# Kernel tuning notes

Measured on AMD Instinct MI355X. Metric: run time of the kernel, lower is better.

## Reference

```python
import jax, jax.numpy as jnp
import numpy as np

N = 50000      # nodes
E = 800000     # edges (before self-loops)
F = 128        # num_features
H = 64         # hidden_channels
B = 512        # batch_size (num graphs)
NC = 10        # num_classes


def setup_inputs() -> dict:
    key = jax.random.key(0)
    ks = jax.random.split(key, 24)
    rn = lambda k, shp, s=0.05: jax.random.normal(k, shp, jnp.float32) * s
    inp = {}
    inp["x"] = jax.random.normal(ks[0], (N, F), jnp.float32)
    inp["edge_index"] = jax.random.randint(ks[1], (2, E), 0, N)
    inp["batch"] = jnp.sort(jax.random.randint(ks[2], (N,), 0, B))
    # GATConv1: in F -> 4 heads x H (concat)
    inp["W1"] = rn(ks[3], (F, 4 * H)); inp["a_src1"] = rn(ks[4], (4, H))
    inp["a_dst1"] = rn(ks[5], (4, H)); inp["b1"] = rn(ks[6], (4 * H,))
    # GATConv2: in 4H -> 1 head x 2H
    inp["W2"] = rn(ks[7], (4 * H, 2 * H)); inp["a_src2"] = rn(ks[8], (1, 2 * H))
    inp["a_dst2"] = rn(ks[9], (1, 2 * H)); inp["b2"] = rn(ks[10], (2 * H,))
    # GCNConv: in 2H -> H
    inp["Wg"] = rn(ks[11], (2 * H, H)); inp["bg"] = rn(ks[12], (H,))
    # BatchNorms (eval mode: running_mean=0, running_var=1)
    inp["bn1_g"] = 1.0 + rn(ks[13], (4 * H,)); inp["bn1_b"] = rn(ks[14], (4 * H,))
    inp["bn2_g"] = 1.0 + rn(ks[15], (2 * H,)); inp["bn2_b"] = rn(ks[16], (2 * H,))
    inp["bn3_g"] = 1.0 + rn(ks[17], (2 * H,)); inp["bn3_b"] = rn(ks[18], (2 * H,))
    inp["lin1_W"] = rn(ks[19], (H, 128)); inp["lin1_b"] = rn(ks[20], (128,))
    inp["lin2_W"] = rn(ks[21], (128, NC)); inp["lin2_b"] = rn(ks[22], (NC,))
    inp["batch_size"] = B
    return inp


def _gat(x, src, dst, W, a_s, a_d, b, n):
    """PyG GATConv (eval): project, edge attention (leaky_relu 0.2), dst-softmax, scatter."""
    heads, ch = a_s.shape
    h = (x @ W).reshape(n, heads, ch)                       # [N, heads, ch]
    sc_s = (h * a_s).sum(-1)                                # [N, heads]
    sc_d = (h * a_d).sum(-1)
    e = jax.nn.leaky_relu(sc_s[src] + sc_d[dst], 0.2)       # [E2, heads]
    m = jax.ops.segment_max(e, dst, num_segments=n)
    ee = jnp.exp(e - m[dst])
    s = jax.ops.segment_sum(ee, dst, num_segments=n)
    alpha = ee / (s[dst] + 1e-16)                           # edge softmax per dst
    out = jax.ops.segment_sum(h[src] * alpha[:, :, None], dst, num_segments=n)
    return out.reshape(n, heads * ch) + b


def _bn_eval(x, g, b, eps=1e-5):
    # BatchNorm1d eval with running_mean=0, running_var=1
    return x * (g / jnp.sqrt(1.0 + eps)) + b


def reference(x, edge_index, batch, W1, a_src1, a_dst1, b1, W2, a_src2, a_dst2, b2,
              Wg, bg, bn1_g, bn1_b, bn2_g, bn2_b, bn3_g, bn3_b,
              lin1_W, lin1_b, lin2_W, lin2_b, batch_size):
    n = x.shape[0]
    loop = jnp.arange(n)
    src = jnp.concatenate([edge_index[0], loop])            # add self-loops (PyG default)
    dst = jnp.concatenate([edge_index[1], loop])
    lrelu = lambda v: jax.nn.leaky_relu(v, 0.01)            # module's LeakyReLU()

    x1 = _bn_eval(lrelu(_gat(x, src, dst, W1, a_src1, a_dst1, b1, n)), bn1_g, bn1_b)
    x2 = _bn_eval(lrelu(_gat(x1, src, dst, W2, a_src2, a_dst2, b2, n)), bn2_g, bn2_b)

    # GCNConv with symmetric normalization over A + I
    deg = jax.ops.segment_sum(jnp.ones_like(dst, jnp.float32), dst, num_segments=n)
    dis = jnp.where(deg > 0, jax.lax.rsqrt(deg), 0.0)
    h = x2 @ Wg                                             # [N, H]
    msg = h[src] * (dis[src] * dis[dst])[:, None]
    x3 = lrelu(jax.ops.segment_sum(msg, dst, num_segments=n) + bg)

    # global_mean_pool over graphs (dropout is identity in eval)
    sums = jax.ops.segment_sum(x3, batch, num_segments=batch_size)
    cnt = jax.ops.segment_sum(jnp.ones((n,), jnp.float32), batch, num_segments=batch_size)
    pooled = sums / jnp.clip(cnt, 1.0)[:, None]             # [B, H]

    y = lrelu(_bn_eval(pooled @ lin1_W + lin1_b, bn3_g, bn3_b))
    return y @ lin2_W + lin2_b                              # [B, NC]
```

## Files before the change

### kernel.cpp

```cpp
#include <hip/hip_runtime.h>
#include <hip/hip_bf16.h>

#define NN  50000
#define EE  800000
#define NE2 850000
#define NB  512
#define NRT 3125
#define NSB 196
#define NEB ((NE2 + 255) / 256)

#define BN_RS 0.9999950000374997f

typedef __attribute__((ext_vector_type(8))) short short8;
typedef __attribute__((ext_vector_type(4))) float f32x4;

__device__ __forceinline__ float bf2f(__hip_bfloat16 v) { return __bfloat162float(v); }
__device__ __forceinline__ unsigned short f2b(float v) {
    __hip_bfloat16 b = __float2bfloat16(v);
    return *reinterpret_cast<unsigned short*>(&b);
}
__device__ __forceinline__ float u2f(unsigned short u) {
    union { unsigned u; float f; } c; c.u = ((unsigned)u) << 16; return c.f;
}
__device__ __forceinline__ float lrelu01(float v) { return v > 0.f ? v : 0.01f * v; }
__device__ __forceinline__ float lrelu02(float v) { return v > 0.f ? v : 0.2f * v; }

__device__ __forceinline__ void up2(unsigned u, float& lo, float& hi) {
    union { unsigned x; float f; } a, b;
    a.x = u << 16; b.x = u & 0xFFFF0000u;
    lo = a.f; hi = b.f;
}
__device__ __forceinline__ void acc8(float* acc, uint4 u, float e) {
    float lo, hi;
    up2(u.x, lo, hi); acc[0] = fmaf(lo, e, acc[0]); acc[1] = fmaf(hi, e, acc[1]);
    up2(u.y, lo, hi); acc[2] = fmaf(lo, e, acc[2]); acc[3] = fmaf(hi, e, acc[3]);
    up2(u.z, lo, hi); acc[4] = fmaf(lo, e, acc[4]); acc[5] = fmaf(hi, e, acc[5]);
    up2(u.w, lo, hi); acc[6] = fmaf(lo, e, acc[6]); acc[7] = fmaf(hi, e, acc[7]);
}
__device__ __forceinline__ unsigned packbf2(float lo, float hi) {
    return ((unsigned)f2b(hi) << 16) | (unsigned)f2b(lo);
}

__device__ __forceinline__ void edge_sd(const int* __restrict__ ei, int e, int& s, int& d) {
    if (e < EE) { s = ei[e]; d = ei[EE + e]; }
    else        { s = e - EE; d = e - EE; }
}

__device__ __forceinline__ float ldf(const void* p, int i, bool bf) {
    return bf ? bf2f(((const __hip_bfloat16*)p)[i]) : ((const float*)p)[i];
}

#define NSEG 20
#define WTOT 85578
#define XQUADS (NN * 32)
#define PREP_TOT (XQUADS + WTOT + 32768 + 32768 + 8192 + NE2)
struct SegArgs { const void* src[NSEG]; int off[NSEG]; };

__global__ __launch_bounds__(256) void prep_k(SegArgs a,
                                              const void* __restrict__ x_raw,
                                              ushort4* __restrict__ xb4,
                                              const void* __restrict__ W1r,
                                              const void* __restrict__ W2r,
                                              const void* __restrict__ Wgr,
                                              float* __restrict__ wf,
                                              unsigned short* __restrict__ W1t,
                                              unsigned short* __restrict__ W2t,
                                              unsigned short* __restrict__ Wgt,
                                              const int* __restrict__ ei,
                                              int* __restrict__ degi,
                                              int* __restrict__ flag) {
    __shared__ int cnt;
    int t = threadIdx.x;
    if (t == 0) cnt = 0;
    __syncthreads();
    {
        int c = 0;
        const unsigned* xw = (const unsigned*)x_raw;
#pragma unroll
        for (int k = 0; k < 4; ++k) {
            unsigned w = xw[t * 4 + k];
            unsigned ef = (w >> 7) & 0xFFu;
            if (ef >= 100u && ef <= 140u) c++;
        }
        atomicAdd(&cnt, c);
    }
    __syncthreads();
    bool bf = (cnt > 512);
    if (blockIdx.x == 0 && t == 0) *flag = bf ? 1 : 0;

    int i = blockIdx.x * 256 + t;
    if (i >= PREP_TOT) return;
    if (i < XQUADS) {
        ushort4 o;
        if (bf) o = ((const ushort4*)x_raw)[i];
        else {
            float4 v = ((const float4*)x_raw)[i];
            o.x = f2b(v.x); o.y = f2b(v.y); o.z = f2b(v.z); o.w = f2b(v.w);
        }
        xb4[i] = o;
        return;
    }
    i -= XQUADS;
    if (i < WTOT) {
        int s = 0;
#pragma unroll
        for (int k = 1; k < NSEG; ++k) if (i >= a.off[k]) s = k;
        wf[i] = ldf(a.src[s], i - a.off[s], bf);
        return;
    }
    i -= WTOT;
    if (i < 32768) {
        int n = i >> 7, k = i & 127;
        W1t[i] = f2b(ldf(W1r, k * 256 + n, bf));
        return;
    }
    i -= 32768;
    if (i < 32768) {
        int n = i >> 8, k = i & 255;
        W2t[i] = f2b(ldf(W2r, k * 128 + n, bf));
        return;
    }
    i -= 32768;
    if (i < 8192) {
        int n = i >> 7, k = i & 127;
        Wgt[i] = f2b(ldf(Wgr, k * 64 + n, bf));
        return;
    }
    i -= 8192;
    {
        int s, d; edge_sd(ei, i, s, d);
        atomicAdd(&degi[d], 1);
    }
}

__global__ __launch_bounds__(256) void pscan_k(const int* __restrict__ degi,
                                               int* __restrict__ incl, int* __restrict__ bsum) {
    __shared__ int tmp[256];
    int t = threadIdx.x;
    int i = blockIdx.x * 256 + t;
    int v = (i < NN) ? degi[i] : 0;
    tmp[t] = v;
    __syncthreads();
#pragma unroll
    for (int off = 1; off < 256; off <<= 1) {
        int u = (t >= off) ? tmp[t - off] : 0;
        __syncthreads();
        tmp[t] += u;
        __syncthreads();
    }
    if (i < NN) incl[i] = tmp[t];
    if (t == 255) bsum[blockIdx.x] = tmp[255];
}

__global__ __launch_bounds__(256) void bscan_k(int* __restrict__ bsum) {
    __shared__ int tmp[256];
    int t = threadIdx.x;
    tmp[t] = (t < NSB) ? bsum[t] : 0;
    __syncthreads();
#pragma unroll
    for (int off = 1; off < 256; off <<= 1) {
        int u = (t >= off) ? tmp[t - off] : 0;
        __syncthreads();
        tmp[t] += u;
        __syncthreads();
    }
    if (t < NSB) bsum[t] = tmp[t];
}

__global__ __launch_bounds__(256) void fscan_k(const int* __restrict__ degi,
                                               const int* __restrict__ incl,
                                               const int* __restrict__ bsum,
                                               const int* __restrict__ batch,
                                               int* __restrict__ row_ptr, int* __restrict__ cursor,
                                               float* __restrict__ dis, int* __restrict__ gstart) {
    int i = blockIdx.x * 256 + threadIdx.x;
    if (i <= NB) {
        int lo = 0, hi = NN;
        while (lo < hi) { int mid = (lo + hi) >> 1; if (batch[mid] < i) lo = mid + 1; else hi = mid; }
        gstart[i] = lo;
    }
    if (i >= NN) return;
    int dg = degi[i];
    int base = (blockIdx.x > 0) ? bsum[blockIdx.x - 1] : 0;
    int ex = base + incl[i] - dg;
    row_ptr[i] = ex; cursor[i] = ex;
    dis[i] = dg > 0 ? rsqrtf((float)dg) : 0.f;
    if (i == NN - 1) row_ptr[NN] = bsum[NSB - 1];
}

__global__ __launch_bounds__(256) void scatter_k(const int* __restrict__ ei,
                                                 int* __restrict__ cursor,
                                                 int* __restrict__ csr_src) {
    int e = blockIdx.x * 256 + threadIdx.x;
    if (e >= NE2) return;
    int s, d; edge_sd(ei, e, s, d);
    int pos = atomicAdd(&cursor[d], 1);
    csr_src[pos] = s;
}

__global__ __launch_bounds__(256) void mgemm1_k(const short* __restrict__ A,
                                                const short* __restrict__ Bt,
                                                unsigned short* __restrict__ C,
                                                const float* __restrict__ a_s,
                                                const float* __restrict__ a_d,
                                                float* __restrict__ sc_s,
                                                float* __restrict__ sc_d) {
    int wave = threadIdx.x >> 6, lane = threadIdx.x & 63;
    int cg = wave;
    int l15 = lane & 15, quad = lane >> 4;
    const short* bp = Bt + (size_t)(cg * 64 + l15) * 128 + quad * 8;
    short8 bfr[4][4];
#pragma unroll
    for (int j = 0; j < 4; ++j)
#pragma unroll
        for (int kk = 0; kk < 4; ++kk)
            bfr[j][kk] = *(const short8*)(bp + (size_t)j * 16 * 128 + kk * 32);
    float asv[4], adv[4];
#pragma unroll
    for (int j = 0; j < 4; ++j) {
        asv[j] = a_s[cg * 64 + j * 16 + l15];
        adv[j] = a_d[cg * 64 + j * 16 + l15];
    }
#pragma unroll
    for (int rtl = 0; rtl < 4; ++rtl) {
        int rt = blockIdx.x * 4 + rtl;
        if (rt >= NRT) break;
        const short* ap = A + (size_t)(rt * 16 + l15) * 128 + quad * 8;
        f32x4 acc[4] = {};
#pragma unroll
        for (int kk = 0; kk < 4; ++kk) {
            short8 a = *(const short8*)(ap + kk * 32);
#pragma unroll
            for (int j = 0; j < 4; ++j)
                acc[j] = __builtin_amdgcn_mfma_f32_16x16x32_bf16(a, bfr[j][kk], acc[j], 0, 0, 0);
        }
        float ss[4] = {0.f, 0.f, 0.f, 0.f}, sd[4] = {0.f, 0.f, 0.f, 0.f};
#pragma unroll
        for (int j = 0; j < 4; ++j) {
            int n = cg * 64 + j * 16 + l15;
#pragma unroll
            for (int r = 0; r < 4; ++r) {
                float v = acc[j][r];
                C[(size_t)(rt * 16 + quad * 4 + r) * 256 + n] = f2b(v);
                ss[r] = fmaf(v, asv[j], ss[r]);
                sd[r] = fmaf(v, adv[j], sd[r]);
            }
        }
#pragma unroll
        for (int off = 1; off < 16; off <<= 1) {
#pragma unroll
            for (int r = 0; r < 4; ++r) {
                ss[r] += __shfl_xor(ss[r], off);
                sd[r] += __shfl_xor(sd[r], off);
            }
        }
        if (l15 == 0) {
#pragma unroll
            for (int r = 0; r < 4; ++r) {
                int node = rt * 16 + quad * 4 + r;
                sc_s[node * 4 + cg] = ss[r];
                sc_d[node * 4 + cg] = sd[r];
            }
        }
    }
}

__global__ __launch_bounds__(256) void mgemm2_k(const short* __restrict__ A,
                                                const short* __restrict__ Bt,
                                                unsigned short* __restrict__ C,
                                                const float* __restrict__ a_s,
                                                const float* __restrict__ a_d,
                                                float* __restrict__ sc_s,
                                                float* __restrict__ sc_d) {
    __shared__ float sred[4][16][2];
    int wave = threadIdx.x >> 6, lane = threadIdx.x & 63;
    int gidx = blockIdx.x * 4 + wave;
    bool act = gidx < NRT * 2;
    int gcl = act ? gidx : NRT * 2 - 1;
    int rt = gcl >> 1, cg = gcl & 1;
    int l15 = lane & 15, quad = lane >> 4;
    const short* ap = A + (size_t)(rt * 16 + l15) * 256 + quad * 8;
    const short* bp = Bt + (size_t)(cg * 64 + l15) * 256 + quad * 8;
    f32x4 acc[4] = {};
    for (int k0 = 0; k0 < 256; k0 += 32) {
        short8 a = *(const short8*)(ap + k0);
#pragma unroll
        for (int j = 0; j < 4; ++j) {
            short8 b = *(const short8*)(bp + (size_t)j * 16 * 256 + k0);
            acc[j] = __builtin_amdgcn_mfma_f32_16x16x32_bf16(a, b, acc[j], 0, 0, 0);
        }
    }
    float asv[4], adv[4];
#pragma unroll
    for (int j = 0; j < 4; ++j) {
        asv[j] = a_s[cg * 64 + j * 16 + l15];
        adv[j] = a_d[cg * 64 + j * 16 + l15];
    }
    float ss[4] = {0.f, 0.f, 0.f, 0.f}, sd[4] = {0.f, 0.f, 0.f, 0.f};
#pragma unroll
    for (int j = 0; j < 4; ++j) {
        int n = cg * 64 + j * 16 + l15;
#pragma unroll
        for (int r = 0; r < 4; ++r) {
            float v = acc[j][r];
            if (act) C[(size_t)(rt * 16 + quad * 4 + r) * 128 + n] = f2b(v);
            ss[r] = fmaf(v, asv[j], ss[r]);
            sd[r] = fmaf(v, adv[j], sd[r]);
        }
    }
#pragma unroll
    for (int off = 1; off < 16; off <<= 1) {
#pragma unroll
        for (int r = 0; r < 4; ++r) {
            ss[r] += __shfl_xor(ss[r], off);
            sd[r] += __shfl_xor(sd[r], off);
        }
    }
    if (l15 == 0) {
#pragma unroll
        for (int r = 0; r < 4; ++r) {
            sred[wave][quad * 4 + r][0] = ss[r];
            sred[wave][quad * 4 + r][1] = sd[r];
        }
    }
    __syncthreads();
    if (threadIdx.x < 32) {
        int rl = threadIdx.x >> 4, row = threadIdx.x & 15;
        int g2 = blockIdx.x * 4 + rl * 2;
        if (g2 < NRT * 2) {
            int node = (g2 >> 1) * 16 + row;
            sc_s[node] = sred[rl * 2][row][0] + sred[rl * 2 + 1][row][0];
            sc_d[node] = sred[rl * 2][row][1] + sred[rl * 2 + 1][row][1];
        }
    }
}

__global__ __launch_bounds__(256) void mgemm3_k(const short* __restrict__ A,
                                                const short* __restrict__ Bt,
                                                unsigned short* __restrict__ C) {
    int wave = threadIdx.x >> 6, lane = threadIdx.x & 63;
    int wt = blockIdx.x * 4 + wave;
    int l15 = lane & 15, quad = lane >> 4;
    const short* bp = Bt + (size_t)l15 * 128 + quad * 8;
    short8 bfr[4][4];
#pragma unroll
    for (int j = 0; j < 4; ++j)
#pragma unroll
        for (int kk = 0; kk < 4; ++kk)
            bfr[j][kk] = *(const short8*)(bp + (size_t)j * 16 * 128 + kk * 32);
#pragma unroll
    for (int rtl = 0; rtl < 4; ++rtl) {
        int rt = wt * 4 + rtl;
        if (rt >= NRT) break;
        const short* ap = A + (size_t)(rt * 16 + l15) * 128 + quad * 8;
        f32x4 acc[4] = {};
#pragma unroll
        for (int kk = 0; kk < 4; ++kk) {
            short8 a = *(const short8*)(ap + kk * 32);
#pragma unroll
            for (int j = 0; j < 4; ++j)
                acc[j] = __builtin_amdgcn_mfma_f32_16x16x32_bf16(a, bfr[j][kk], acc[j], 0, 0, 0);
        }
#pragma unroll
        for (int j = 0; j < 4; ++j) {
            int n = j * 16 + l15;
#pragma unroll
            for (int r = 0; r < 4; ++r)
                C[(size_t)(rt * 16 + quad * 4 + r) * 64 + n] = f2b(acc[j][r]);
        }
    }
}

__device__ __forceinline__ float sel4(float4 v, int head) {
    float ab = (head & 1) ? v.y : v.x;
    float cd = (head & 1) ? v.w : v.z;
    return (head & 2) ? cd : ab;
}

__global__ __launch_bounds__(256) void agg1_k(const int* __restrict__ row_ptr,
                                              const int* __restrict__ csr_src,
                                              const uint4* __restrict__ h1b,
                                              const float* __restrict__ sc_s,
                                              const float4* __restrict__ sc_d4,
                                              const float4* __restrict__ b1,
                                              const float4* __restrict__ g1,
                                              const float4* __restrict__ bb1,
                                              uint4* __restrict__ x1b) {
    int n = __builtin_amdgcn_readfirstlane((blockIdx.x * 256 + threadIdx.x) >> 6);
    int lane = threadIdx.x & 63;
    if (n >= NN) return;
    int g = lane >> 5, sl = lane & 31;
    int head = sl >> 3;
    int row = row_ptr[n], end = row_ptr[n + 1];
    float scd_h = sel4(sc_d4[n], head);
    float acc[8] = {0.f, 0.f, 0.f, 0.f, 0.f, 0.f, 0.f, 0.f};
    float den = 0.f;
    int c = row;
    for (; c + 7 < end; c += 8) {
        int i0 = c + g, i1 = c + 2 + g, i2 = c + 4 + g, i3 = c + 6 + g;
        int s0 = csr_src[i0], s1 = csr_src[i1], s2 = csr_src[i2], s3 = csr_src[i3];
        float w0 = sc_s[s0 * 4 + head], w1 = sc_s[s1 * 4 + head];
        float w2 = sc_s[s2 * 4 + head], w3 = sc_s[s3 * 4 + head];
        uint4 u0 = h1b[(size_t)s0 * 32 + sl];
        uint4 u1 = h1b[(size_t)s1 * 32 + sl];
        uint4 u2 = h1b[(size_t)s2 * 32 + sl];
        uint4 u3 = h1b[(size_t)s3 * 32 + sl];
        float e0 = __expf(lrelu02(w0 + scd_h));
        float e1 = __expf(lrelu02(w1 + scd_h));
        float e2 = __expf(lrelu02(w2 + scd_h));
        float e3 = __expf(lrelu02(w3 + scd_h));
        den += (e0 + e1) + (e2 + e3);
        acc8(acc, u0, e0); acc8(acc, u1, e1); acc8(acc, u2, e2); acc8(acc, u3, e3);
    }
    for (int cc = c + g; cc < end; cc += 2) {
        int s0 = csr_src[cc];
        float e0 = __expf(lrelu02(sc_s[s0 * 4 + head] + scd_h));
        uint4 u0 = h1b[(size_t)s0 * 32 + sl];
        den += e0;
        acc8(acc, u0, e0);
    }
    den += __shfl_xor(den, 32);
#pragma unroll
    for (int k = 0; k < 8; ++k) acc[k] += __shfl_xor(acc[k], 32);
    if (g == 0) {
        float inv = 1.f / (den + 1e-16f);
        float4 bA = b1[sl * 2],  bB = b1[sl * 2 + 1];
        float4 gA = g1[sl * 2],  gB = g1[sl * 2 + 1];
        float4 eA = bb1[sl * 2], eB = bb1[sl * 2 + 1];
        float o0 = lrelu01(fmaf(acc[0], inv, bA.x)) * (gA.x * BN_RS) + eA.x;
        float o1 = lrelu01(fmaf(acc[1], inv, bA.y)) * (gA.y * BN_RS) + eA.y;
        float o2 = lrelu01(fmaf(acc[2], inv, bA.z)) * (gA.z * BN_RS) + eA.z;
        float o3 = lrelu01(fmaf(acc[3], inv, bA.w)) * (gA.w * BN_RS) + eA.w;
        float o4 = lrelu01(fmaf(acc[4], inv, bB.x)) * (gB.x * BN_RS) + eB.x;
        float o5 = lrelu01(fmaf(acc[5], inv, bB.y)) * (gB.y * BN_RS) + eB.y;
        float o6 = lrelu01(fmaf(acc[6], inv, bB.z)) * (gB.z * BN_RS) + eB.z;
        float o7 = lrelu01(fmaf(acc[7], inv, bB.w)) * (gB.w * BN_RS) + eB.w;
        uint4 w;
        w.x = packbf2(o0, o1); w.y = packbf2(o2, o3);
        w.z = packbf2(o4, o5); w.w = packbf2(o6, o7);
        x1b[(size_t)n * 32 + sl] = w;
    }
}

__global__ __launch_bounds__(256) void agg2_k(const int* __restrict__ row_ptr,
                                              const int* __restrict__ csr_src,
                                              const uint4* __restrict__ h2b,
                                              const float* __restrict__ sc_s,
                                              const float* __restrict__ sc_d,
                                              const float4* __restrict__ b2,
                                              const float4* __restrict__ g2,
                                              const float4* __restrict__ bb2,
                                              uint4* __restrict__ x2b) {
    int n = __builtin_amdgcn_readfirstlane((blockIdx.x * 256 + threadIdx.x) >> 6);
    int lane = threadIdx.x & 63;
    if (n >= NN) return;
    int g = lane >> 4, sl = lane & 15;
    int row = row_ptr[n], end = row_ptr[n + 1];
    float scd = sc_d[n];
    float acc[8] = {0.f, 0.f, 0.f, 0.f, 0.f, 0.f, 0.f, 0.f};
    float den = 0.f;
    int c = row + g;
    for (; c + 12 < end; c += 16) {
        int s0 = csr_src[c], s1 = csr_src[c + 4], s2 = csr_src[c + 8], s3 = csr_src[c + 12];
        float c0 = sc_s[s0], c1 = sc_s[s1], c2 = sc_s[s2], c3 = sc_s[s3];
        uint4 u0 = h2b[(size_t)s0 * 16 + sl];
        uint4 u1 = h2b[(size_t)s1 * 16 + sl];
        uint4 u2 = h2b[(size_t)s2 * 16 + sl];
        uint4 u3 = h2b[(size_t)s3 * 16 + sl];
        float e0 = __expf(lrelu02(c0 + scd));
        float e1 = __expf(lrelu02(c1 + scd));
        float e2 = __expf(lrelu02(c2 + scd));
        float e3 = __expf(lrelu02(c3 + scd));
        den += (e0 + e1) + (e2 + e3);
        acc8(acc, u0, e0); acc8(acc, u1, e1); acc8(acc, u2, e2); acc8(acc, u3, e3);
    }
    for (; c < end; c += 4) {
        int s0 = csr_src[c];
        float e0 = __expf(lrelu02(sc_s[s0] + scd));
        uint4 u0 = h2b[(size_t)s0 * 16 + sl];
        den += e0;
        acc8(acc, u0, e0);
    }
    den += __shfl_xor(den, 16);
    den += __shfl_xor(den, 32);
#pragma unroll
    for (int k = 0; k < 8; ++k) {
        acc[k] += __shfl_xor(acc[k], 16);
        acc[k] += __shfl_xor(acc[k], 32);
    }
    if (lane < 16) {
        float inv = 1.f / (den + 1e-16f);
        float4 bA = b2[sl * 2],  bB = b2[sl * 2 + 1];
        float4 gA = g2[sl * 2],  gB = g2[sl * 2 + 1];
        float4 eA = bb2[sl * 2], eB = bb2[sl * 2 + 1];
        float o0 = lrelu01(fmaf(acc[0], inv, bA.x)) * (gA.x * BN_RS) + eA.x;
        float o1 = lrelu01(fmaf(acc[1], inv, bA.y)) * (gA.y * BN_RS) + eA.y;
        float o2 = lrelu01(fmaf(acc[2], inv, bA.z)) * (gA.z * BN_RS) + eA.z;
        float o3 = lrelu01(fmaf(acc[3], inv, bA.w)) * (gA.w * BN_RS) + eA.w;
        float o4 = lrelu01(fmaf(acc[4], inv, bB.x)) * (gB.x * BN_RS) + eB.x;
        float o5 = lrelu01(fmaf(acc[5], inv, bB.y)) * (gB.y * BN_RS) + eB.y;
        float o6 = lrelu01(fmaf(acc[6], inv, bB.z)) * (gB.z * BN_RS) + eB.z;
        float o7 = lrelu01(fmaf(acc[7], inv, bB.w)) * (gB.w * BN_RS) + eB.w;
        uint4 w;
        w.x = packbf2(o0, o1); w.y = packbf2(o2, o3);
        w.z = packbf2(o4, o5); w.w = packbf2(o6, o7);
        x2b[(size_t)n * 16 + sl] = w;
    }
}

__global__ __launch_bounds__(256) void gcn_k(const int* __restrict__ row_ptr,
                                             const int* __restrict__ csr_src,
                                             const uint4* __restrict__ hgb,
                                             const float* __restrict__ dis,
                                             const float4* __restrict__ bg,
                                             float4* __restrict__ x3) {
    int n = __builtin_amdgcn_readfirstlane((blockIdx.x * 256 + threadIdx.x) >> 6);
    int lane = threadIdx.x & 63;
    if (n >= NN) return;
    int g = lane >> 3, sl = lane & 7;
    int row = row_ptr[n], end = row_ptr[n + 1];
    float dn = dis[n];
    float acc[8] = {0.f, 0.f, 0.f, 0.f, 0.f, 0.f, 0.f, 0.f};
    int c = row + g;
    for (; c + 8 < end; c += 16) {
        int s0 = csr_src[c], s1 = csr_src[c + 8];
        float w0 = dis[s0], w1 = dis[s1];
        uint4 u0 = hgb[(size_t)s0 * 8 + sl];
        uint4 u1 = hgb[(size_t)s1 * 8 + sl];
        acc8(acc, u0, w0); acc8(acc, u1, w1);
    }
    for (; c < end; c += 8) {
        int s0 = csr_src[c];
        float w0 = dis[s0];
        uint4 u0 = hgb[(size_t)s0 * 8 + sl];
        acc8(acc, u0, w0);
    }
#pragma unroll
    for (int off = 8; off <= 32; off <<= 1) {
#pragma unroll
        for (int k = 0; k < 8; ++k) acc[k] += __shfl_xor(acc[k], off);
    }
    if (lane < 8) {
        float4 bA = bg[sl * 2], bB = bg[sl * 2 + 1];
        float4 oA, oB;
        oA.x = lrelu01(fmaf(acc[0], dn, bA.x));
        oA.y = lrelu01(fmaf(acc[1], dn, bA.y));
        oA.z = lrelu01(fmaf(acc[2], dn, bA.z));
        oA.w = lrelu01(fmaf(acc[3], dn, bA.w));
        oB.x = lrelu01(fmaf(acc[4], dn, bB.x));
        oB.y = lrelu01(fmaf(acc[5], dn, bB.y));
        oB.z = lrelu01(fmaf(acc[6], dn, bB.z));
        oB.w = lrelu01(fmaf(acc[7], dn, bB.w));
        x3[(size_t)n * 16 + sl * 2]     = oA;
        x3[(size_t)n * 16 + sl * 2 + 1] = oB;
    }
}

__global__ __launch_bounds__(256) void poolmlp_k(const float* __restrict__ x3,
                                                 const int* __restrict__ gstart,
                                                 const float* __restrict__ l1W,
                                                 const float* __restrict__ l1b,
                                                 const float* __restrict__ g3,
                                                 const float* __restrict__ b3,
                                                 const float* __restrict__ l2W,
                                                 const float* __restrict__ l2b,
                                                 void* __restrict__ outp,
                                                 const int* __restrict__ flag) {
    __shared__ float red[4][64];
    __shared__ float pl[64];
    __shared__ float y1s[128];
    int g = blockIdx.x, t = threadIdx.x;
    int c = t & 63, r = t >> 6;
    int s = gstart[g], e = gstart[g + 1];
    float sum = 0.f;
    for (int n = s + r; n < e; n += 4) sum += x3[(size_t)n * 64 + c];
    red[r][c] = sum;
    __syncthreads();
    if (t < 64) {
        float v = red[0][t] + red[1][t] + red[2][t] + red[3][t];
        int cnt = e - s; if (cnt < 1) cnt = 1;
        pl[t] = v / (float)cnt;
    }
    __syncthreads();
    if (t < 128) {
        float acc = l1b[t];
#pragma unroll 8
        for (int j = 0; j < 64; ++j) acc = fmaf(pl[j], l1W[j * 128 + t], acc);
        acc = acc * (g3[t] * BN_RS) + b3[t];
        y1s[t] = lrelu01(acc);
    }
    __syncthreads();
    if (t < 10) {
        float o = l2b[t];
#pragma unroll 8
        for (int j = 0; j < 128; ++j) o = fmaf(y1s[j], l2W[j * 10 + t], o);
        if (*flag) ((__hip_bfloat16*)outp)[g * 10 + t] = __float2bfloat16(o);
        else       ((float*)outp)[g * 10 + t] = o;
    }
}

static const int kSegN[NSEG]  = {32768, 256, 256, 256, 32768, 128, 128, 128, 8192, 64,
                                 256, 256, 128, 128, 128, 128, 8192, 128, 1280, 10};
static const int kSegIn[NSEG] = {3, 4, 5, 6, 7, 8, 9, 10, 11, 12, 13, 14, 15, 16, 17, 18, 19, 20, 21, 22};

extern "C" void kernel_launch(void* const* d_in, const int* in_sizes, int n_in,
                              void* d_out, int out_size, void* d_ws, size_t ws_size,
                              hipStream_t stream) {
    const void* x_raw = d_in[0];
    const int*  ei    = (const int*)d_in[1];
    const int*  batch = (const int*)d_in[2];

    int*   flag = (int*)d_ws;
    float* ws   = (float*)d_ws;
    unsigned short* xb = (unsigned short*)(ws + 16);
    float* wf   = ws + 16 + (size_t)NN * 64;
    unsigned short* W1t = (unsigned short*)(wf + 85584);
    unsigned short* W2t = W1t + 32768;
    unsigned short* Wgt = W2t + 32768;
    unsigned short* h1b = Wgt + 8192;
    unsigned short* x1b = h1b + (size_t)NN * 256;
    unsigned short* x2b = x1b + (size_t)NN * 256;
    unsigned short* hgb = x2b + (size_t)NN * 128;
    float* x3   = (float*)(hgb + (size_t)NN * 64);
    float* sc_s1 = x3 + (size_t)NN * 64;
    float* sc_d1 = sc_s1 + (size_t)NN * 4;
    float* sc_s2 = sc_d1 + (size_t)NN * 4;
    float* sc_d2 = sc_s2 + NN;
    float* disb  = sc_d2 + NN;
    int*   gstart = (int*)(disb + NN);
    int*   degi   = gstart + NB + 4;
    int*   incl   = degi + NN;
    int*   bsum   = incl + NN;
    int*   row_ptr = bsum + 256;
    int*   cursor  = row_ptr + NN + 1;
    int*   csr_src = cursor + NN;

    int off[NSEG]; int o = 0;
    for (int s = 0; s < NSEG; ++s) { off[s] = o; o += kSegN[s]; }
    float* as1f = wf + off[1];  float* ad1f = wf + off[2];
    float* b1f  = wf + off[3];  float* as2f = wf + off[5];
    float* ad2f = wf + off[6];  float* b2f  = wf + off[7];
    float* bgf  = wf + off[9];  float* bn1g = wf + off[10]; float* bn1b = wf + off[11];
    float* bn2g = wf + off[12]; float* bn2b = wf + off[13]; float* bn3g = wf + off[14];
    float* bn3b = wf + off[15]; float* l1Wf = wf + off[16]; float* l1bf = wf + off[17];
    float* l2Wf = wf + off[18]; float* l2bf = wf + off[19];

    unsigned short* h2b = h1b;

    hipMemsetAsync(degi, 0, NN * sizeof(int), stream);
    SegArgs sa;
    for (int s = 0; s < NSEG; ++s) { sa.src[s] = d_in[kSegIn[s]]; sa.off[s] = off[s]; }
    prep_k<<<(PREP_TOT + 255) / 256, 256, 0, stream>>>(sa, x_raw, (ushort4*)xb,
                                                       d_in[3], d_in[7], d_in[11],
                                                       wf, W1t, W2t, Wgt, ei, degi, flag);

    pscan_k<<<NSB, 256, 0, stream>>>(degi, incl, bsum);
    bscan_k<<<1, 256, 0, stream>>>(bsum);
    fscan_k<<<NSB, 256, 0, stream>>>(degi, incl, bsum, batch, row_ptr, cursor, disb, gstart);
    scatter_k<<<NEB, 256, 0, stream>>>(ei, cursor, csr_src);

    mgemm1_k<<<(NRT + 3) / 4, 256, 0, stream>>>((const short*)xb, (const short*)W1t, h1b,
                                                as1f, ad1f, sc_s1, sc_d1);
    agg1_k<<<12500, 256, 0, stream>>>(row_ptr, csr_src, (const uint4*)h1b,
                                      sc_s1, (const float4*)sc_d1,
                                      (const float4*)b1f, (const float4*)bn1g,
                                      (const float4*)bn1b, (uint4*)x1b);

    mgemm2_k<<<(NRT * 2 + 3) / 4, 256, 0, stream>>>((const short*)x1b, (const short*)W2t, h2b,
                                                    as2f, ad2f, sc_s2, sc_d2);
    agg2_k<<<12500, 256, 0, stream>>>(row_ptr, csr_src, (const uint4*)h2b,
                                      sc_s2, sc_d2,
                                      (const float4*)b2f, (const float4*)bn2g,
                                      (const float4*)bn2b, (uint4*)x2b);

    mgemm3_k<<<(NRT + 15) / 16, 256, 0, stream>>>((const short*)x2b, (const short*)Wgt, hgb);
    gcn_k<<<12500, 256, 0, stream>>>(row_ptr, csr_src, (const uint4*)hgb, disb,
                                     (const float4*)bgf, (float4*)x3);
    poolmlp_k<<<NB, 256, 0, stream>>>(x3, gstart, l1Wf, l1bf, bn3g, bn3b, l2Wf, l2bf,
                                      d_out, flag);
}
```

Before: 426.7 us.

## Store projected features head-major and split aggregation waves per head/feature slice

```diff
diff --git a/kernel.cpp b/kernel.cpp
--- a/kernel.cpp
+++ b/kernel.cpp
@@ -237,11 +237,12 @@
         float ss[4] = {0.f, 0.f, 0.f, 0.f}, sd[4] = {0.f, 0.f, 0.f, 0.f};
 #pragma unroll
         for (int j = 0; j < 4; ++j) {
-            int n = cg * 64 + j * 16 + l15;
+            int f = j * 16 + l15;
 #pragma unroll
             for (int r = 0; r < 4; ++r) {
                 float v = acc[j][r];
-                C[(size_t)(rt * 16 + quad * 4 + r) * 256 + n] = f2b(v);
+                int m = rt * 16 + quad * 4 + r;
+                C[((size_t)cg * NN + m) * 64 + f] = f2b(v);
                 ss[r] = fmaf(v, asv[j], ss[r]);
                 sd[r] = fmaf(v, adv[j], sd[r]);
             }
@@ -299,11 +300,12 @@
     float ss[4] = {0.f, 0.f, 0.f, 0.f}, sd[4] = {0.f, 0.f, 0.f, 0.f};
 #pragma unroll
     for (int j = 0; j < 4; ++j) {
-        int n = cg * 64 + j * 16 + l15;
+        int f = j * 16 + l15;
 #pragma unroll
         for (int r = 0; r < 4; ++r) {
             float v = acc[j][r];
-            if (act) C[(size_t)(rt * 16 + quad * 4 + r) * 128 + n] = f2b(v);
+            int m = rt * 16 + quad * 4 + r;
+            if (act) C[((size_t)cg * NN + m) * 64 + f] = f2b(v);
             ss[r] = fmaf(v, asv[j], ss[r]);
             sd[r] = fmaf(v, adv[j], sd[r]);
         }
@@ -363,70 +365,71 @@
         }
 #pragma unroll
         for (int j = 0; j < 4; ++j) {
-            int n = j * 16 + l15;
-#pragma unroll
-            for (int r = 0; r < 4; ++r)
-                C[(size_t)(rt * 16 + quad * 4 + r) * 64 + n] = f2b(acc[j][r]);
-        }
-    }
-}
-
-__device__ __forceinline__ float sel4(float4 v, int head) {
-    float ab = (head & 1) ? v.y : v.x;
-    float cd = (head & 1) ? v.w : v.z;
-    return (head & 2) ? cd : ab;
+            int nf = j * 16 + l15;
+            int fb = nf >> 5, wf2 = nf & 31;
+#pragma unroll
+            for (int r = 0; r < 4; ++r) {
+                int m = rt * 16 + quad * 4 + r;
+                C[((size_t)fb * NN + m) * 32 + wf2] = f2b(acc[j][r]);
+            }
+        }
+    }
 }
 
 __global__ __launch_bounds__(256) void agg1_k(const int* __restrict__ row_ptr,
                                               const int* __restrict__ csr_src,
-                                              const uint4* __restrict__ h1b,
+                                              const uint4* __restrict__ h1hm,
                                               const float* __restrict__ sc_s,
-                                              const float4* __restrict__ sc_d4,
+                                              const float* __restrict__ sc_d,
                                               const float4* __restrict__ b1,
                                               const float4* __restrict__ g1,
                                               const float4* __restrict__ bb1,
                                               uint4* __restrict__ x1b) {
-    int n = __builtin_amdgcn_readfirstlane((blockIdx.x * 256 + threadIdx.x) >> 6);
+    int wid = __builtin_amdgcn_readfirstlane((blockIdx.x * 256 + threadIdx.x) >> 6);
     int lane = threadIdx.x & 63;
-    if (n >= NN) return;
-    int g = lane >> 5, sl = lane & 31;
-    int head = sl >> 3;
+    if (wid >= 4 * NN) return;
+    int h = wid / NN;
+    int n = wid - h * NN;
+    int g = lane >> 3, sl = lane & 7;
     int row = row_ptr[n], end = row_ptr[n + 1];
-    float scd_h = sel4(sc_d4[n], head);
+    float scd_h = sc_d[n * 4 + h];
+    const uint4* tab = h1hm + (size_t)h * NN * 8;
     float acc[8] = {0.f, 0.f, 0.f, 0.f, 0.f, 0.f, 0.f, 0.f};
     float den = 0.f;
     int c = row;
-    for (; c + 7 < end; c += 8) {
-        int i0 = c + g, i1 = c + 2 + g, i2 = c + 4 + g, i3 = c + 6 + g;
-        int s0 = csr_src[i0], s1 = csr_src[i1], s2 = csr_src[i2], s3 = csr_src[i3];
-        float w0 = sc_s[s0 * 4 + head], w1 = sc_s[s1 * 4 + head];
-        float w2 = sc_s[s2 * 4 + head], w3 = sc_s[s3 * 4 + head];
-        uint4 u0 = h1b[(size_t)s0 * 32 + sl];
-        uint4 u1 = h1b[(size_t)s1 * 32 + sl];
-        uint4 u2 = h1b[(size_t)s2 * 32 + sl];
-        uint4 u3 = h1b[(size_t)s3 * 32 + sl];
+    for (; c + 15 < end; c += 16) {
+        int i0 = c + g, i1 = c + 8 + g;
+        int s0 = csr_src[i0], s1 = csr_src[i1];
+        float w0 = sc_s[s0 * 4 + h], w1 = sc_s[s1 * 4 + h];
+        uint4 u0 = tab[(size_t)s0 * 8 + sl];
+        uint4 u1 = tab[(size_t)s1 * 8 + sl];
         float e0 = __expf(lrelu02(w0 + scd_h));
         float e1 = __expf(lrelu02(w1 + scd_h));
-        float e2 = __expf(lrelu02(w2 + scd_h));
-        float e3 = __expf(lrelu02(w3 + scd_h));
-        den += (e0 + e1) + (e2 + e3);
-        acc8(acc, u0, e0); acc8(acc, u1, e1); acc8(acc, u2, e2); acc8(acc, u3, e3);
-    }
-    for (int cc = c + g; cc < end; cc += 2) {
+        den += e0 + e1;
+        acc8(acc, u0, e0); acc8(acc, u1, e1);
+    }
+    for (int cc = c + g; cc < end; cc += 8) {
         int s0 = csr_src[cc];
-        float e0 = __expf(lrelu02(sc_s[s0 * 4 + head] + scd_h));
-        uint4 u0 = h1b[(size_t)s0 * 32 + sl];
+        float e0 = __expf(lrelu02(sc_s[s0 * 4 + h] + scd_h));
+        uint4 u0 = tab[(size_t)s0 * 8 + sl];
         den += e0;
         acc8(acc, u0, e0);
     }
+    den += __shfl_xor(den, 8);
+    den += __shfl_xor(den, 16);
     den += __shfl_xor(den, 32);
 #pragma unroll
-    for (int k = 0; k < 8; ++k) acc[k] += __shfl_xor(acc[k], 32);
+    for (int k = 0; k < 8; ++k) {
+        acc[k] += __shfl_xor(acc[k], 8);
+        acc[k] += __shfl_xor(acc[k], 16);
+        acc[k] += __shfl_xor(acc[k], 32);
+    }
     if (g == 0) {
         float inv = 1.f / (den + 1e-16f);
-        float4 bA = b1[sl * 2],  bB = b1[sl * 2 + 1];
-        float4 gA = g1[sl * 2],  gB = g1[sl * 2 + 1];
-        float4 eA = bb1[sl * 2], eB = bb1[sl * 2 + 1];
+        int pb = h * 16 + sl * 2;
+        float4 bA = b1[pb],  bB = b1[pb + 1];
+        float4 gA = g1[pb],  gB = g1[pb + 1];
+        float4 eA = bb1[pb], eB = bb1[pb + 1];
         float o0 = lrelu01(fmaf(acc[0], inv, bA.x)) * (gA.x * BN_RS) + eA.x;
         float o1 = lrelu01(fmaf(acc[1], inv, bA.y)) * (gA.y * BN_RS) + eA.y;
         float o2 = lrelu01(fmaf(acc[2], inv, bA.z)) * (gA.z * BN_RS) + eA.z;
@@ -438,61 +441,64 @@
         uint4 w;
         w.x = packbf2(o0, o1); w.y = packbf2(o2, o3);
         w.z = packbf2(o4, o5); w.w = packbf2(o6, o7);
-        x1b[(size_t)n * 32 + sl] = w;
+        x1b[(size_t)n * 32 + h * 8 + sl] = w;
     }
 }
 
 __global__ __launch_bounds__(256) void agg2_k(const int* __restrict__ row_ptr,
                                               const int* __restrict__ csr_src,
-                                              const uint4* __restrict__ h2b,
+                                              const uint4* __restrict__ h2fm,
                                               const float* __restrict__ sc_s,
                                               const float* __restrict__ sc_d,
                                               const float4* __restrict__ b2,
                                               const float4* __restrict__ g2,
                                               const float4* __restrict__ bb2,
                                               uint4* __restrict__ x2b) {
-    int n = __builtin_amdgcn_readfirstlane((blockIdx.x * 256 + threadIdx.x) >> 6);
+    int wid = __builtin_amdgcn_readfirstlane((blockIdx.x * 256 + threadIdx.x) >> 6);
     int lane = threadIdx.x & 63;
-    if (n >= NN) return;
-    int g = lane >> 4, sl = lane & 15;
+    if (wid >= 2 * NN) return;
+    int f = wid / NN;
+    int n = wid - f * NN;
+    int g = lane >> 3, sl = lane & 7;
     int row = row_ptr[n], end = row_ptr[n + 1];
     float scd = sc_d[n];
+    const uint4* tab = h2fm + (size_t)f * NN * 8;
     float acc[8] = {0.f, 0.f, 0.f, 0.f, 0.f, 0.f, 0.f, 0.f};
     float den = 0.f;
-    int c = row + g;
-    for (; c + 12 < end; c += 16) {
-        int s0 = csr_src[c], s1 = csr_src[c + 4], s2 = csr_src[c + 8], s3 = csr_src[c + 12];
-        float c0 = sc_s[s0], c1 = sc_s[s1], c2 = sc_s[s2], c3 = sc_s[s3];
-        uint4 u0 = h2b[(size_t)s0 * 16 + sl];
-        uint4 u1 = h2b[(size_t)s1 * 16 + sl];
-        uint4 u2 = h2b[(size_t)s2 * 16 + sl];
-        uint4 u3 = h2b[(size_t)s3 * 16 + sl];
-        float e0 = __expf(lrelu02(c0 + scd));
-        float e1 = __expf(lrelu02(c1 + scd));
-        float e2 = __expf(lrelu02(c2 + scd));
-        float e3 = __expf(lrelu02(c3 + scd));
-        den += (e0 + e1) + (e2 + e3);
-        acc8(acc, u0, e0); acc8(acc, u1, e1); acc8(acc, u2, e2); acc8(acc, u3, e3);
-    }
-    for (; c < end; c += 4) {
-        int s0 = csr_src[c];
+    int c = row;
+    for (; c + 15 < end; c += 16) {
+        int i0 = c + g, i1 = c + 8 + g;
+        int s0 = csr_src[i0], s1 = csr_src[i1];
+        float w0 = sc_s[s0], w1 = sc_s[s1];
+        uint4 u0 = tab[(size_t)s0 * 8 + sl];
+        uint4 u1 = tab[(size_t)s1 * 8 + sl];
+        float e0 = __expf(lrelu02(w0 + scd));
+        float e1 = __expf(lrelu02(w1 + scd));
+        den += e0 + e1;
+        acc8(acc, u0, e0); acc8(acc, u1, e1);
+    }
+    for (int cc = c + g; cc < end; cc += 8) {
+        int s0 = csr_src[cc];
         float e0 = __expf(lrelu02(sc_s[s0] + scd));
-        uint4 u0 = h2b[(size_t)s0 * 16 + sl];
+        uint4 u0 = tab[(size_t)s0 * 8 + sl];
         den += e0;
         acc8(acc, u0, e0);
     }
+    den += __shfl_xor(den, 8);
     den += __shfl_xor(den, 16);
     den += __shfl_xor(den, 32);
 #pragma unroll
     for (int k = 0; k < 8; ++k) {
+        acc[k] += __shfl_xor(acc[k], 8);
         acc[k] += __shfl_xor(acc[k], 16);
         acc[k] += __shfl_xor(acc[k], 32);
     }
-    if (lane < 16) {
+    if (g == 0) {
         float inv = 1.f / (den + 1e-16f);
-        float4 bA = b2[sl * 2],  bB = b2[sl * 2 + 1];
-        float4 gA = g2[sl * 2],  gB = g2[sl * 2 + 1];
-        float4 eA = bb2[sl * 2], eB = bb2[sl * 2 + 1];
+        int pb = f * 16 + sl * 2;
+        float4 bA = b2[pb],  bB = b2[pb + 1];
+        float4 gA = g2[pb],  gB = g2[pb + 1];
+        float4 eA = bb2[pb], eB = bb2[pb + 1];
         float o0 = lrelu01(fmaf(acc[0], inv, bA.x)) * (gA.x * BN_RS) + eA.x;
         float o1 = lrelu01(fmaf(acc[1], inv, bA.y)) * (gA.y * BN_RS) + eA.y;
         float o2 = lrelu01(fmaf(acc[2], inv, bA.z)) * (gA.z * BN_RS) + eA.z;
@@ -504,44 +510,48 @@
         uint4 w;
         w.x = packbf2(o0, o1); w.y = packbf2(o2, o3);
         w.z = packbf2(o4, o5); w.w = packbf2(o6, o7);
-        x2b[(size_t)n * 16 + sl] = w;
+        x2b[(size_t)n * 16 + f * 8 + sl] = w;
     }
 }
 
 __global__ __launch_bounds__(256) void gcn_k(const int* __restrict__ row_ptr,
                                              const int* __restrict__ csr_src,
-                                             const uint4* __restrict__ hgb,
+                                             const uint4* __restrict__ hgfm,
                                              const float* __restrict__ dis,
                                              const float4* __restrict__ bg,
                                              float4* __restrict__ x3) {
-    int n = __builtin_amdgcn_readfirstlane((blockIdx.x * 256 + threadIdx.x) >> 6);
+    int wid = __builtin_amdgcn_readfirstlane((blockIdx.x * 256 + threadIdx.x) >> 6);
     int lane = threadIdx.x & 63;
-    if (n >= NN) return;
-    int g = lane >> 3, sl = lane & 7;
+    if (wid >= 2 * NN) return;
+    int f = wid / NN;
+    int n = wid - f * NN;
+    int g = lane >> 2, sl = lane & 3;
     int row = row_ptr[n], end = row_ptr[n + 1];
     float dn = dis[n];
+    const uint4* tab = hgfm + (size_t)f * NN * 4;
     float acc[8] = {0.f, 0.f, 0.f, 0.f, 0.f, 0.f, 0.f, 0.f};
-    int c = row + g;
-    for (; c + 8 < end; c += 16) {
-        int s0 = csr_src[c], s1 = csr_src[c + 8];
-        float w0 = dis[s0], w1 = dis[s1];
-        uint4 u0 = hgb[(size_t)s0 * 8 + sl];
-        uint4 u1 = hgb[(size_t)s1 * 8 + sl];
-        acc8(acc, u0, w0); acc8(acc, u1, w1);
-    }
-    for (; c < end; c += 8) {
-        int s0 = csr_src[c];
+    int c = row;
+    for (; c + 15 < end; c += 16) {
+        int i0 = c + g;
+        int s0 = csr_src[i0];
         float w0 = dis[s0];
-        uint4 u0 = hgb[(size_t)s0 * 8 + sl];
+        uint4 u0 = tab[(size_t)s0 * 4 + sl];
         acc8(acc, u0, w0);
     }
-#pragma unroll
-    for (int off = 8; off <= 32; off <<= 1) {
+    for (int cc = c + g; cc < end; cc += 16) {
+        int s0 = csr_src[cc];
+        float w0 = dis[s0];
+        uint4 u0 = tab[(size_t)s0 * 4 + sl];
+        acc8(acc, u0, w0);
+    }
+#pragma unroll
+    for (int off = 4; off <= 32; off <<= 1) {
 #pragma unroll
         for (int k = 0; k < 8; ++k) acc[k] += __shfl_xor(acc[k], off);
     }
-    if (lane < 8) {
-        float4 bA = bg[sl * 2], bB = bg[sl * 2 + 1];
+    if (g == 0) {
+        int pb = f * 8 + sl * 2;
+        float4 bA = bg[pb], bB = bg[pb + 1];
         float4 oA, oB;
         oA.x = lrelu01(fmaf(acc[0], dn, bA.x));
         oA.y = lrelu01(fmaf(acc[1], dn, bA.y));
@@ -551,8 +561,8 @@
         oB.y = lrelu01(fmaf(acc[5], dn, bB.y));
         oB.z = lrelu01(fmaf(acc[6], dn, bB.z));
         oB.w = lrelu01(fmaf(acc[7], dn, bB.w));
-        x3[(size_t)n * 16 + sl * 2]     = oA;
-        x3[(size_t)n * 16 + sl * 2 + 1] = oB;
+        x3[(size_t)n * 16 + pb]     = oA;
+        x3[(size_t)n * 16 + pb + 1] = oB;
     }
 }
 
@@ -661,20 +671,20 @@
 
     mgemm1_k<<<(NRT + 3) / 4, 256, 0, stream>>>((const short*)xb, (const short*)W1t, h1b,
                                                 as1f, ad1f, sc_s1, sc_d1);
-    agg1_k<<<12500, 256, 0, stream>>>(row_ptr, csr_src, (const uint4*)h1b,
-                                      sc_s1, (const float4*)sc_d1,
+    agg1_k<<<50000, 256, 0, stream>>>(row_ptr, csr_src, (const uint4*)h1b,
+                                      sc_s1, sc_d1,
                                       (const float4*)b1f, (const float4*)bn1g,
                                       (const float4*)bn1b, (uint4*)x1b);
 
     mgemm2_k<<<(NRT * 2 + 3) / 4, 256, 0, stream>>>((const short*)x1b, (const short*)W2t, h2b,
                                                     as2f, ad2f, sc_s2, sc_d2);
-    agg2_k<<<12500, 256, 0, stream>>>(row_ptr, csr_src, (const uint4*)h2b,
+    agg2_k<<<25000, 256, 0, stream>>>(row_ptr, csr_src, (const uint4*)h2b,
                                       sc_s2, sc_d2,
                                       (const float4*)b2f, (const float4*)bn2g,
                                       (const float4*)bn2b, (uint4*)x2b);
 
     mgemm3_k<<<(NRT + 15) / 16, 256, 0, stream>>>((const short*)x2b, (const short*)Wgt, hgb);
-    gcn_k<<<12500, 256, 0, stream>>>(row_ptr, csr_src, (const uint4*)hgb, disb,
+    gcn_k<<<25000, 256, 0, stream>>>(row_ptr, csr_src, (const uint4*)hgb, disb,
                                      (const float4*)bgf, (float4*)x3);
     poolmlp_k<<<NB, 256, 0, stream>>>(x3, gstart, l1Wf, l1bf, bn3g, bn3b, l2Wf, l2bf,
                                       d_out, flag);
```

Result: slower. 473.5 us (+11.0%).
